# Kernel tuning notes

Hardware: AMD Instinct MI355X
Metric: run time of the kernel (lower is better)

## Reference

```python
import jax, jax.numpy as jnp
import numpy as np

DIM = 1024
SEQ_LEN = 2048
NUM_HEAD = 16
HEAD_DIM = 64
B = 4


def setup_inputs() -> dict:
    key = jax.random.key(0)
    ks = jax.random.split(key, 9)
    hd = NUM_HEAD * HEAD_DIM
    s_in = 1.0 / np.sqrt(DIM)
    s_o = 1.0 / np.sqrt(hd)
    return {
        "x": jax.random.normal(ks[0], (B, SEQ_LEN, DIM), dtype=jnp.float32),
        "q_w": jax.random.uniform(ks[1], (hd, DIM), jnp.float32, -s_in, s_in),
        "q_b": jax.random.uniform(ks[2], (hd,), jnp.float32, -s_in, s_in),
        "k_w": jax.random.uniform(ks[3], (hd, DIM), jnp.float32, -s_in, s_in),
        "k_b": jax.random.uniform(ks[4], (hd,), jnp.float32, -s_in, s_in),
        "v_w": jax.random.uniform(ks[5], (hd, DIM), jnp.float32, -s_in, s_in),
        "v_b": jax.random.uniform(ks[6], (hd,), jnp.float32, -s_in, s_in),
        "o_w": jax.random.uniform(ks[7], (DIM, hd), jnp.float32, -s_o, s_o),
        "o_b": jax.random.uniform(ks[8], (DIM,), jnp.float32, -s_o, s_o),
    }


def reference(x, q_w, q_b, k_w, k_b, v_w, v_b, o_w, o_b):
    Bn, T, C = x.shape
    # QKV projections (torch Linear: x @ W^T + b)
    q = (x @ q_w.T + q_b).reshape(Bn, T, NUM_HEAD, HEAD_DIM).transpose(0, 2, 1, 3)
    k = (x @ k_w.T + k_b).reshape(Bn, T, NUM_HEAD, HEAD_DIM).transpose(0, 2, 1, 3)
    v = (x @ v_w.T + v_b).reshape(Bn, T, NUM_HEAD, HEAD_DIM).transpose(0, 2, 1, 3)
    scale = HEAD_DIM ** -0.5
    attn = jnp.einsum("bhqd,bhkd->bhqk", q, k) * scale  # (B,H,T,T)
    causal = jnp.tril(jnp.ones((T, T), dtype=bool))
    attn = jnp.where(causal[None, None, :, :], attn, -jnp.inf)
    p = jax.nn.softmax(attn, axis=-1)  # stable softmax (max-subtracted)
    out = jnp.einsum("bhqk,bhkd->bhqd", p, v)
    out = out.transpose(0, 2, 1, 3).reshape(Bn, T, NUM_HEAD * HEAD_DIM)
    return out @ o_w.T + o_b
```

## Files before the change

kernel.cpp:

```cpp
#include <hip/hip_runtime.h>
#include <stdint.h>

typedef short short8 __attribute__((ext_vector_type(8)));
typedef float f32x4 __attribute__((ext_vector_type(4)));
typedef float f32x16 __attribute__((ext_vector_type(16)));
typedef unsigned int uint2v __attribute__((ext_vector_type(2)));
typedef unsigned int uint4v __attribute__((ext_vector_type(4)));

__device__ __forceinline__ unsigned short f2bf(float f) {
    unsigned int u = __float_as_uint(f);
    u += 0x7fffu + ((u >> 16) & 1u);
    return (unsigned short)(u >> 16);
}

__device__ __forceinline__ void gld_lds16(const unsigned short* g, unsigned short* l) {
    __builtin_amdgcn_global_load_lds((const __attribute__((address_space(1))) unsigned int*)g,
                                     (__attribute__((address_space(3))) unsigned int*)l,
                                     16, 0, 0);
}

#define QSCL 0.18033688011112042f

__global__ __launch_bounds__(256) void cvt_all(const float* __restrict__ x,
                                               const float* __restrict__ qw, const float* __restrict__ kw,
                                               const float* __restrict__ vw, const float* __restrict__ ow,
                                               const float* __restrict__ qb, const float* __restrict__ kb,
                                               const float* __restrict__ vb,
                                               unsigned short* __restrict__ Xb,
                                               unsigned short* __restrict__ Wqkv,
                                               unsigned short* __restrict__ Owb,
                                               float* __restrict__ bqkv) {
    int i = blockIdx.x * 256 + threadIdx.x;
    const float* src; uint2* dst; int j;
    if (i < 2097152)      { src = x;  dst = (uint2*)Xb;                j = i; }
    else if (i < 2359296) { src = qw; dst = (uint2*)Wqkv;              j = i - 2097152; }
    else if (i < 2621440) { src = kw; dst = (uint2*)(Wqkv + 1048576);  j = i - 2359296; }
    else if (i < 2883584) { src = vw; dst = (uint2*)(Wqkv + 2097152);  j = i - 2621440; }
    else if (i < 3145728) { src = ow; dst = (uint2*)Owb;               j = i - 2883584; }
    else {
        int t = i - 3145728;
        const float4* bs = (t < 256) ? (const float4*)qb : (t < 512) ? (const float4*)kb : (const float4*)vb;
        ((float4*)bqkv)[t] = bs[t & 255];
        return;
    }
    float4 v = ((const float4*)src)[j];
    unsigned int lo = (unsigned int)f2bf(v.x) | ((unsigned int)f2bf(v.y) << 16);
    unsigned int hi = (unsigned int)f2bf(v.z) | ((unsigned int)f2bf(v.w) << 16);
    dst[j] = make_uint2(lo, hi);
}

template<int MODE>
__global__ __launch_bounds__(256) void gemm_bt(const unsigned short* __restrict__ A,
                                               const unsigned short* __restrict__ Bm,
                                               const float* __restrict__ bias,
                                               void* __restrict__ C0,
                                               unsigned short* __restrict__ VtOut,
                                               int M, int N, int K)
{
    __shared__ __align__(16) unsigned short As[128 * 64];
    __shared__ __align__(16) unsigned short Bs[128 * 64];
    const int tid  = threadIdx.x;
    const int bm   = blockIdx.x, bn = blockIdx.y;
    const int lane = tid & 63, w = tid >> 6;
    const int wm   = w >> 1, wn = w & 1;
    const int quad = lane >> 4, l15 = lane & 15;

    f32x4 acc[4][4];
#pragma unroll
    for (int mt = 0; mt < 4; mt++)
#pragma unroll
        for (int nt = 0; nt < 4; nt++)
            acc[mt][nt] = (f32x4){0.f, 0.f, 0.f, 0.f};

    const int kTiles = K >> 6;
    for (int kt = 0; kt < kTiles; ++kt) {
        __syncthreads();
#pragma unroll
        for (int i = 0; i < 4; i++) {
            int G  = i * 256 + tid;
            int m  = G >> 3, g = G & 7;
            int gs = g ^ (m & 7);
            int Gb = i * 256 + (w << 6);
            gld_lds16(A  + (size_t)(bm * 128 + m) * K + kt * 64 + gs * 8, &As[Gb * 8]);
            gld_lds16(Bm + (size_t)(bn * 128 + m) * K + kt * 64 + gs * 8, &Bs[Gb * 8]);
        }
        __syncthreads();
#pragma unroll
        for (int ks = 0; ks < 2; ++ks) {
            short8 af[4], bfr[4];
#pragma unroll
            for (int mt = 0; mt < 4; mt++) {
                int m = wm * 64 + mt * 16 + l15;
                af[mt] = *(const short8*)&As[m * 64 + (((ks * 4 + quad) ^ (l15 & 7)) << 3)];
            }
#pragma unroll
            for (int nt = 0; nt < 4; nt++) {
                int n = wn * 64 + nt * 16 + l15;
                bfr[nt] = *(const short8*)&Bs[n * 64 + (((ks * 4 + quad) ^ (l15 & 7)) << 3)];
            }
#pragma unroll
            for (int mt = 0; mt < 4; mt++)
#pragma unroll
                for (int nt = 0; nt < 4; nt++)
                    acc[mt][nt] = __builtin_amdgcn_mfma_f32_16x16x32_bf16(af[mt], bfr[nt], acc[mt][nt], 0, 0, 0);
        }
    }
    const int row0 = bm * 128 + wm * 64, col0 = bn * 128 + wn * 64;
#pragma unroll
    for (int nt = 0; nt < 4; nt++) {
        int col = col0 + nt * 16 + l15;
        float bv = bias[col];
#pragma unroll
        for (int mt = 0; mt < 4; mt++) {
            if (MODE == 1 && col >= 2048) {
                int row = row0 + mt * 16 + quad * 4;
                int b = row >> 11, t = row & 2047;
                ushort4 pk;
                pk.x = f2bf(acc[mt][nt][0] + bv);
                pk.y = f2bf(acc[mt][nt][1] + bv);
                pk.z = f2bf(acc[mt][nt][2] + bv);
                pk.w = f2bf(acc[mt][nt][3] + bv);
                *(ushort4*)(VtOut + (size_t)(b * 1024 + (col - 2048)) * 2048 + t) = pk;
            } else {
#pragma unroll
                for (int r = 0; r < 4; r++) {
                    int row = row0 + mt * 16 + quad * 4 + r;
                    float v = acc[mt][nt][r] + bv;
                    if (MODE == 1) {
                        if (col < 1024) v *= QSCL;
                        ((unsigned short*)C0)[(size_t)row * 2048 + col] = f2bf(v);
                    } else {
                        ((float*)C0)[(size_t)row * N + col] = v;
                    }
                }
            }
        }
    }
}

#define NEG_RAW (-1e30f)
__global__ __launch_bounds__(512, 4) void attn_mfma(const unsigned short* __restrict__ QK,
                                                    const unsigned short* __restrict__ Vt,
                                                    unsigned short* __restrict__ O)
{
    __shared__ __align__(16) unsigned short Kb[3][64 * 64];
    __shared__ __align__(16) unsigned short Vb[3][64 * 64];
    const int tid  = threadIdx.x;
    const int lane = tid & 63, w = tid >> 6;
    const int hi   = lane >> 5, l31 = lane & 31;
    const int s7   = lane & 7;
    const int bid  = (int)blockIdx.x;
    const int bh   = bid & 63;
    const int G    = bid >> 6;
    const int qt   = (G < 4) ? (7 - G) : (G - 4);
    const int b    = bh >> 4, h = bh & 15;
    const int qbase = qt * 256 + w * 32;

    const unsigned short* Qp = QK + (size_t)(b * 2048) * 2048 + h * 64;
    const unsigned short* Kp = Qp + 1024;
    const unsigned short* Vp = Vt + (size_t)(bh * 64) * 2048;

    short8 qf[4];
    {
        const unsigned short* qrow = Qp + (size_t)(qbase + l31) * 2048 + hi * 8;
#pragma unroll
        for (int dk = 0; dk < 4; dk++)
            qf[dk] = *(const short8*)(qrow + dk * 16);
    }

    f32x16 oacc[2];
#pragma unroll
    for (int i = 0; i < 2; i++)
#pragma unroll
        for (int r = 0; r < 16; r++) oacc[i][r] = 0.f;
    float lsum = 0.f;

    const int ktend   = 4 * qt + 3;
    const int ktmax_w = (qbase + 31) >> 6;

    auto stage = [&](int t, int bi) {
        int r = tid >> 3, g = tid & 7, gs = g ^ (r & 7);
        gld_lds16(Kp + (size_t)(t * 64 + r) * 2048 + gs * 8, &Kb[bi][w * 512]);
        gld_lds16(Vp + (size_t)r * 2048 + t * 64 + gs * 8, &Vb[bi][w * 512]);
    };

    stage(0, 0);
    stage(1, 1);

    int cur = 0;
    for (int kt = 0; kt <= ktend; ++kt) {
        if (kt < ktend) asm volatile("s_waitcnt vmcnt(2)" ::: "memory");
        else            asm volatile("s_waitcnt vmcnt(0)" ::: "memory");
        __builtin_amdgcn_sched_barrier(0);
        __builtin_amdgcn_s_barrier();
        __builtin_amdgcn_sched_barrier(0);
        if (kt + 2 <= ktend) {
            int bi = cur + 2; if (bi >= 3) bi -= 3;
            stage(kt + 2, bi);
        }
        if (kt <= ktmax_w) {
            __builtin_amdgcn_s_setprio(1);
            const unsigned short* Kc = Kb[cur];
            const unsigned short* Vc = Vb[cur];
            const int kbase = kt * 64;
#pragma unroll
            for (int sub = 0; sub < 2; sub++) {
                const int kb0 = kbase + sub * 32;
                if (kb0 > qbase + 31) continue;
                f32x16 sacc;
#pragma unroll
                for (int r = 0; r < 16; r++) sacc[r] = 0.f;
                const unsigned short* kr = &Kc[(sub * 32 + l31) * 64];
#pragma unroll
                for (int dk = 0; dk < 4; dk++) {
                    short8 kf = *(const short8*)(kr + (((dk * 2 + hi) ^ s7) << 3));
                    sacc = __builtin_amdgcn_mfma_f32_32x32x16_bf16(kf, qf[dk], sacc, 0, 0, 0);
                }
                if (kb0 + 31 > qbase) {
                    const int qg = qbase + l31;
                    const int kb = kb0 + 4 * hi;
#pragma unroll
                    for (int r = 0; r < 16; r++) {
                        int key = kb + (r & 3) + 8 * (r >> 2);
                        if (key > qg) sacc[r] = NEG_RAW;
                    }
                }
#pragma unroll
                for (int r = 0; r < 16; r++) sacc[r] = __builtin_exp2f(sacc[r]);
                {
                    float s0 = (sacc[0] + sacc[1]) + (sacc[2] + sacc[3]);
                    float s1 = (sacc[4] + sacc[5]) + (sacc[6] + sacc[7]);
                    float s2 = (sacc[8] + sacc[9]) + (sacc[10] + sacc[11]);
                    float s3 = (sacc[12] + sacc[13]) + (sacc[14] + sacc[15]);
                    lsum += (s0 + s1) + (s2 + s3);
                }
                unsigned int pk[8];
#pragma unroll
                for (int t2 = 0; t2 < 8; t2++)
                    pk[t2] = __builtin_amdgcn_perm(__float_as_uint(sacc[2 * t2 + 1]),
                                                   __float_as_uint(sacc[2 * t2]), 0x07060302u);
                uint2v r0 = __builtin_amdgcn_permlane32_swap(pk[0], pk[2], false, false);
                uint2v r1 = __builtin_amdgcn_permlane32_swap(pk[1], pk[3], false, false);
                uint2v r2 = __builtin_amdgcn_permlane32_swap(pk[4], pk[6], false, false);
                uint2v r3 = __builtin_amdgcn_permlane32_swap(pk[5], pk[7], false, false);
                short8 pf[2];
                { uint4v u; u.x = r0.x; u.y = r1.x; u.z = r0.y; u.w = r1.y; pf[0] = __builtin_bit_cast(short8, u); }
                { uint4v u; u.x = r2.x; u.y = r3.x; u.z = r2.y; u.w = r3.y; pf[1] = __builtin_bit_cast(short8, u); }
#pragma unroll
                for (int kv = 0; kv < 2; kv++) {
#pragma unroll
                    for (int dsub = 0; dsub < 2; dsub++) {
                        const int d = dsub * 32 + l31;
                        short8 vf = *(const short8*)&Vc[d * 64 + (((sub * 4 + kv * 2 + hi) ^ s7) << 3)];
                        oacc[dsub] = __builtin_amdgcn_mfma_f32_32x32x16_bf16(vf, pf[kv], oacc[dsub], 0, 0, 0);
                    }
                }
            }
            __builtin_amdgcn_s_setprio(0);
        }
        cur = (cur == 2) ? 0 : cur + 1;
    }

    uint2v lt = __builtin_amdgcn_permlane32_swap(__float_as_uint(lsum), __float_as_uint(lsum), false, false);
    const float inv = 1.f / (__uint_as_float(lt.x) + __uint_as_float(lt.y));
    unsigned short* op = O + (size_t)(b * 2048 + qbase + l31) * 1024 + h * 64;
#pragma unroll
    for (int dsub = 0; dsub < 2; dsub++) {
#pragma unroll
        for (int q4 = 0; q4 < 4; q4++) {
            ushort4 pkv;
            pkv.x = f2bf(oacc[dsub][q4 * 4 + 0] * inv);
            pkv.y = f2bf(oacc[dsub][q4 * 4 + 1] * inv);
            pkv.z = f2bf(oacc[dsub][q4 * 4 + 2] * inv);
            pkv.w = f2bf(oacc[dsub][q4 * 4 + 3] * inv);
            *(ushort4*)(op + dsub * 32 + q4 * 8 + hi * 4) = pkv;
        }
    }
}

extern "C" void kernel_launch(void* const* d_in, const int* in_sizes, int n_in,
                              void* d_out, int out_size, void* d_ws, size_t ws_size,
                              hipStream_t stream)
{
    const float* x   = (const float*)d_in[0];
    const float* q_w = (const float*)d_in[1];
    const float* q_b = (const float*)d_in[2];
    const float* k_w = (const float*)d_in[3];
    const float* k_b = (const float*)d_in[4];
    const float* v_w = (const float*)d_in[5];
    const float* v_b = (const float*)d_in[6];
    const float* o_w = (const float*)d_in[7];
    const float* o_b = (const float*)d_in[8];
    float* out = (float*)d_out;

    unsigned short* Xb   = (unsigned short*)d_ws;
    unsigned short* Wqkv = Xb + 8388608;
    unsigned short* Owb  = Wqkv + 3145728;
    float*          bqkv = (float*)(Owb + 1048576);
    unsigned short* QK   = (unsigned short*)(bqkv + 3072);
    unsigned short* Vtg  = QK + 16777216;
    unsigned short* Abf  = Vtg + 8388608;

    cvt_all<<<12291, 256, 0, stream>>>(x, q_w, k_w, v_w, o_w, q_b, k_b, v_b,
                                       Xb, Wqkv, Owb, bqkv);
    gemm_bt<1><<<dim3(64, 24), 256, 0, stream>>>(Xb, Wqkv, bqkv, QK, Vtg, 8192, 3072, 1024);
    attn_mfma<<<512, 512, 0, stream>>>(QK, Vtg, Abf);
    gemm_bt<0><<<dim3(64, 8), 256, 0, stream>>>(Abf, Owb, o_b, out, nullptr, 8192, 1024, 1024);
}
```

Measured before the change: 260.0 us.

## Split attention KV range across wave pairs with LDS reduction, smaller query tiles

Each attention block now covers 128 query rows instead of 256. The 8 waves form two groups, and each group handles alternating 64-key tiles, so waves process KV tiles in parallel rather than each wave holding its own query rows. Tiles are staged in pairs into a 4-deep LDS buffer, and the partial output accumulators and row sums are combined through LDS at the end. This doubles the grid and is meant to shorten the per-block critical path and balance causal work better. The cost is an extra barrier per iteration and an LDS reduction epilogue. The code relies on the softmax running without a running-max rescale, so partial sums can simply be added.

```diff
diff --git a/kernel.cpp b/kernel.cpp
--- a/kernel.cpp
+++ b/kernel.cpp
@@ -143,18 +143,18 @@
                                                     const unsigned short* __restrict__ Vt,
                                                     unsigned short* __restrict__ O)
 {
-    __shared__ __align__(16) unsigned short Kb[3][64 * 64];
-    __shared__ __align__(16) unsigned short Vb[3][64 * 64];
+    __shared__ __align__(16) unsigned short Kb[4][64 * 64];
+    __shared__ __align__(16) unsigned short Vb[4][64 * 64];
     const int tid  = threadIdx.x;
     const int lane = tid & 63, w = tid >> 6;
+    const int ws   = w & 3;
+    const int par  = w >> 2;
     const int hi   = lane >> 5, l31 = lane & 31;
     const int s7   = lane & 7;
-    const int bid  = (int)blockIdx.x;
-    const int bh   = bid & 63;
-    const int G    = bid >> 6;
-    const int qt   = (G < 4) ? (7 - G) : (G - 4);
+    const int bh   = blockIdx.x;
     const int b    = bh >> 4, h = bh & 15;
-    const int qbase = qt * 256 + w * 32;
+    const int qt   = (int)gridDim.y - 1 - (int)blockIdx.y;
+    const int qbase = qt * 128 + ws * 32;
 
     const unsigned short* Qp = QK + (size_t)(b * 2048) * 2048 + h * 64;
     const unsigned short* Kp = Qp + 1024;
@@ -175,33 +175,35 @@
         for (int r = 0; r < 16; r++) oacc[i][r] = 0.f;
     float lsum = 0.f;
 
-    const int ktend   = 4 * qt + 3;
+    const int np      = qt + 1;
     const int ktmax_w = (qbase + 31) >> 6;
 
-    auto stage = [&](int t, int bi) {
+    auto stageT = [&](int t, int bi) {
         int r = tid >> 3, g = tid & 7, gs = g ^ (r & 7);
         gld_lds16(Kp + (size_t)(t * 64 + r) * 2048 + gs * 8, &Kb[bi][w * 512]);
         gld_lds16(Vp + (size_t)r * 2048 + t * 64 + gs * 8, &Vb[bi][w * 512]);
     };
-
-    stage(0, 0);
-    stage(1, 1);
-
-    int cur = 0;
-    for (int kt = 0; kt <= ktend; ++kt) {
-        if (kt < ktend) asm volatile("s_waitcnt vmcnt(2)" ::: "memory");
+    auto stageP = [&](int p) {
+        int bp = (p & 1) << 1;
+        stageT(2 * p, bp);
+        stageT(2 * p + 1, bp + 1);
+    };
+
+    stageP(0);
+    if (np > 1) stageP(1);
+
+    for (int p = 0; p < np; ++p) {
+        const int bp = (p & 1) << 1;
+        if (p < np - 1) asm volatile("s_waitcnt vmcnt(4)" ::: "memory");
         else            asm volatile("s_waitcnt vmcnt(0)" ::: "memory");
         __builtin_amdgcn_sched_barrier(0);
         __builtin_amdgcn_s_barrier();
         __builtin_amdgcn_sched_barrier(0);
-        if (kt + 2 <= ktend) {
-            int bi = cur + 2; if (bi >= 3) bi -= 3;
-            stage(kt + 2, bi);
-        }
+        const int kt = 2 * p + par;
         if (kt <= ktmax_w) {
             __builtin_amdgcn_s_setprio(1);
-            const unsigned short* Kc = Kb[cur];
-            const unsigned short* Vc = Vb[cur];
+            const unsigned short* Kc = Kb[bp + par];
+            const unsigned short* Vc = Vb[bp + par];
             const int kbase = kt * 64;
 #pragma unroll
             for (int sub = 0; sub < 2; sub++) {
@@ -258,22 +260,44 @@
             }
             __builtin_amdgcn_s_setprio(0);
         }
-        cur = (cur == 2) ? 0 : cur + 1;
-    }
-
-    uint2v lt = __builtin_amdgcn_permlane32_swap(__float_as_uint(lsum), __float_as_uint(lsum), false, false);
-    const float inv = 1.f / (__uint_as_float(lt.x) + __uint_as_float(lt.y));
-    unsigned short* op = O + (size_t)(b * 2048 + qbase + l31) * 1024 + h * 64;
-#pragma unroll
-    for (int dsub = 0; dsub < 2; dsub++) {
-#pragma unroll
-        for (int q4 = 0; q4 < 4; q4++) {
-            ushort4 pkv;
-            pkv.x = f2bf(oacc[dsub][q4 * 4 + 0] * inv);
-            pkv.y = f2bf(oacc[dsub][q4 * 4 + 1] * inv);
-            pkv.z = f2bf(oacc[dsub][q4 * 4 + 2] * inv);
-            pkv.w = f2bf(oacc[dsub][q4 * 4 + 3] * inv);
-            *(ushort4*)(op + dsub * 32 + q4 * 8 + hi * 4) = pkv;
+        __builtin_amdgcn_sched_barrier(0);
+        __builtin_amdgcn_s_barrier();
+        __builtin_amdgcn_sched_barrier(0);
+        if (p + 2 < np) stageP(p + 2);
+    }
+
+    float* cb = (float*)&Kb[0][0];
+    const int cbase = ws * 2112;
+    if (par == 1) {
+#pragma unroll
+        for (int dsub = 0; dsub < 2; dsub++)
+#pragma unroll
+            for (int r = 0; r < 16; r++)
+                cb[cbase + (dsub * 16 + r) * 64 + lane] = oacc[dsub][r];
+        cb[cbase + 32 * 64 + lane] = lsum;
+    }
+    __syncthreads();
+    if (par == 0) {
+#pragma unroll
+        for (int dsub = 0; dsub < 2; dsub++)
+#pragma unroll
+            for (int r = 0; r < 16; r++)
+                oacc[dsub][r] += cb[cbase + (dsub * 16 + r) * 64 + lane];
+        lsum += cb[cbase + 32 * 64 + lane];
+        uint2v lt = __builtin_amdgcn_permlane32_swap(__float_as_uint(lsum), __float_as_uint(lsum), false, false);
+        const float inv = 1.f / (__uint_as_float(lt.x) + __uint_as_float(lt.y));
+        unsigned short* op = O + (size_t)(b * 2048 + qbase + l31) * 1024 + h * 64;
+#pragma unroll
+        for (int dsub = 0; dsub < 2; dsub++) {
+#pragma unroll
+            for (int q4 = 0; q4 < 4; q4++) {
+                ushort4 pkv;
+                pkv.x = f2bf(oacc[dsub][q4 * 4 + 0] * inv);
+                pkv.y = f2bf(oacc[dsub][q4 * 4 + 1] * inv);
+                pkv.z = f2bf(oacc[dsub][q4 * 4 + 2] * inv);
+                pkv.w = f2bf(oacc[dsub][q4 * 4 + 3] * inv);
+                *(ushort4*)(op + dsub * 32 + q4 * 8 + hi * 4) = pkv;
+            }
         }
     }
 }
@@ -304,6 +328,6 @@
     cvt_all<<<12291, 256, 0, stream>>>(x, q_w, k_w, v_w, o_w, q_b, k_b, v_b,
                                        Xb, Wqkv, Owb, bqkv);
     gemm_bt<1><<<dim3(64, 24), 256, 0, stream>>>(Xb, Wqkv, bqkv, QK, Vtg, 8192, 3072, 1024);
-    attn_mfma<<<512, 512, 0, stream>>>(QK, Vtg, Abf);
+    attn_mfma<<<dim3(64, 16), 512, 0, stream>>>(QK, Vtg, Abf);
     gemm_bt<0><<<dim3(64, 8), 256, 0, stream>>>(Abf, Owb, o_b, out, nullptr, 8192, 1024, 1024);
 }
```

Result: no change. 256.0 us (-1.5%).
